# Kernel optimization log

Measured on AMD Instinct MI355X. Metric: run time of the kernel, lower is better.

Reference implementation:

```python
import jax, jax.numpy as jnp
import numpy as np

PI = jnp.pi


def _spow(t, p):
    # t >= 0; safe t**p with value 0 (and zero grad) at t == 0
    tt = jnp.where(t > 0, t, 1.0)
    return jnp.where(t > 0, tt ** p, 0.0)


def _wavelets(t, f, fm, pm, em, fo, ph):
    # t: [L]; f: [S,1] -> returns [S, L] bank of wavelets (one per scale)
    sigma = jnp.maximum(fm / (2.0 * PI * f), 1e-6)        # [S,1]
    br = jnp.cos(2.0 * PI * f * t)                        # [S,L]
    bi = jnp.sin(2.0 * PI * f * t)
    # real_part: + pm0*br - c^2 (t/sig)^fo0 br pm1 + ... alternating, c = 2..7
    real = br * pm[0]
    sign = -1.0
    for j in range(6):
        c = j + 2.0
        real = real + sign * (_spow(t, fo[j]) * c / sigma ** fo[j] * c) * br * pm[j + 1]
        sign = -sign
    # imag_part: same pattern with fo6..fo11, pm8..pm13; j==9 term has the
    # anomalous parenthesization from the source: t**fo*5/(sigma**fo*5)
    imag = bi * pm[7]
    sign = -1.0
    for j in range(6, 12):
        c = j - 4.0
        if j == 9:
            term = (_spow(t, fo[j]) * 5.0 / (sigma ** fo[j] * 5.0)) * bi * pm[j + 2]
        else:
            term = (_spow(t, fo[j]) * c / sigma ** fo[j] * c) * bi * pm[j + 2]
        imag = imag + sign * term
        sign = -sign
    gauss = em[0] * jnp.exp(-t ** 2 / (2.0 * sigma ** 2))  # [S,L]
    rw = real * gauss
    iw = imag * gauss
    amp = rw + iw
    samp = amp / jnp.linalg.norm(amp, axis=-1, keepdims=True)
    phase = jnp.arctan2(iw, rw)
    w = (samp * jnp.sin(phase) * ph[0]) * (samp * jnp.cos(phase) * ph[1]) \
        * (samp * jnp.sinc(phase / PI) * ph[2])
    return w


def reference(x, scales, f_mod, poly_mod, exp_mod, frac_order, phase_mod, i):
    B, C = x.shape[0], x.shape[1]
    xf = x.reshape(B, C, -1)                              # [B,C,L]
    L = xf.shape[-1]
    S = scales.shape[0]
    t = jnp.arange(L, dtype=x.dtype)
    f = (1.0 / scales)[:, None]                           # [S,1]
    W = _wavelets(t, f, f_mod[i], poly_mod[i], exp_mod[i], frac_order[i],
                  phase_mod[i])                            # [S,L] kernels, K = L
    # torch F.conv1d(padding='same', groups=C*S) = cross-correlation with
    # left pad (K-1)//2. Computed exactly via zero-padded FFT linear conv.
    K = L
    Nfft = 2 * L                                          # >= L + K - 1, no aliasing
    Xf = jnp.fft.rfft(xf, n=Nfft, axis=-1)                # [B,C,F]
    Wf = jnp.fft.rfft(W[:, ::-1], n=Nfft, axis=-1)        # [S,F] (corr = conv w/ flip)
    y = jnp.fft.irfft(Xf[:, :, None, :] * Wf[None, None], n=Nfft, axis=-1)  # [B,C,S,2L]
    left = (K - 1) // 2
    off = K - 1 - left
    y = y[..., off:off + L]                               # [B,C,S,L]
    # torch channel layout: out[:, j] = corr(x[:, j % C], wavelet[j % S])
    j = jnp.arange(C * S)
    return y[:, j % C, j % S, :]                          # [B, C*S, L]


def setup_inputs() -> dict:
    key = jax.random.key(0)
    ks = jax.random.split(key, 6)
    B, C, H, Wd = 16, 16, 64, 64
    S, NSTEPS = 16, 10
    x = jax.random.normal(ks[0], (B, C, H, Wd), dtype=jnp.float32)
    scales = jnp.linspace(1.0, 32.0, S, dtype=jnp.float32)
    f_mod = 1.0 + 0.02 * jax.random.normal(ks[1], (NSTEPS,), dtype=jnp.float32)
    poly_mod = 1.0 + 0.02 * jax.random.normal(ks[2], (NSTEPS, 14), dtype=jnp.float32)
    exp_mod = 1.0 + 0.02 * jax.random.normal(ks[3], (NSTEPS, 1), dtype=jnp.float32)
    frac_order = 1.0 + 0.02 * jax.random.normal(ks[4], (NSTEPS, 12), dtype=jnp.float32)
    phase_mod = 1.0 + 0.02 * jax.random.normal(ks[5], (NSTEPS, 3), dtype=jnp.float32)
    return {"x": x, "scales": scales, "f_mod": f_mod, "poly_mod": poly_mod,
            "exp_mod": exp_mod, "frac_order": frac_order,
            "phase_mod": phase_mod, "i": 3}
```

## Files before the change

kernel.cpp:

```cpp
#include <hip/hip_runtime.h>
#include <math.h>

#define QMAX 128
#define ZCUT 1920
#define PAD  131

__global__ void wavelet_build(const float* __restrict__ scales,
                              const float* __restrict__ f_mod,
                              const float* __restrict__ poly_mod,
                              const float* __restrict__ exp_mod,
                              const float* __restrict__ frac_order,
                              const float* __restrict__ phase_mod,
                              const int* __restrict__ istep,
                              float* __restrict__ Wout) {
    const int k = blockIdx.x;
    const int t = threadIdx.x;
    const int i = istep[0];
    const float PI2 = 6.28318530717958647692f;

    const float scale = scales[k];
    const float f = 1.0f / scale;
    const float fm = f_mod[i];
    const float* pm = poly_mod + i * 14;
    const float em0 = exp_mod[i];
    const float* fo = frac_order + i * 12;
    const float* ph = phase_mod + i * 3;

    const float sigma = fmaxf(fm / (PI2 * f), 1e-6f);
    const float tf = (float)t;
    const float arg = PI2 * f * tf;
    const float br = cosf(arg);
    const float bi = sinf(arg);

    float rp = pm[0];
    float sign = -1.0f;
    for (int j = 0; j < 6; ++j) {
        float c = (float)(j + 2);
        float sp = (tf > 0.0f) ? powf(tf, fo[j]) : 0.0f;
        float term = sp * c / powf(sigma, fo[j]) * c * pm[j + 1];
        rp += sign * term;
        sign = -sign;
    }
    float ipoly = pm[7];
    sign = -1.0f;
    for (int j = 6; j < 12; ++j) {
        float sp = (tf > 0.0f) ? powf(tf, fo[j]) : 0.0f;
        float term;
        if (j == 9) {
            term = sp * 5.0f / (powf(sigma, fo[j]) * 5.0f) * pm[j + 2];
        } else {
            float c = (float)(j - 4);
            term = sp * c / powf(sigma, fo[j]) * c * pm[j + 2];
        }
        ipoly += sign * term;
        sign = -sign;
    }

    const float gauss = em0 * expf(-tf * tf / (2.0f * sigma * sigma));
    const float rw = br * rp * gauss;
    const float iw = bi * ipoly * gauss;
    const float amp = rw + iw;

    float sq = amp * amp;
    #pragma unroll
    for (int off = 32; off > 0; off >>= 1) sq += __shfl_xor(sq, off, 64);
    __shared__ float wsum[2];
    if ((t & 63) == 0) wsum[t >> 6] = sq;
    __syncthreads();
    const float norm = sqrtf(wsum[0] + wsum[1]);

    const float samp = amp / norm;
    const float phase = atan2f(iw, rw);
    const float sphi = sinf(phase);
    const float cphi = cosf(phase);
    const float snc = (phase != 0.0f) ? (sphi / phase) : 1.0f;
    const float w = (samp * sphi * ph[0]) * (samp * cphi * ph[1]) * (samp * snc * ph[2]);
    Wout[k * QMAX + t] = w;
}

__global__ __launch_bounds__(256) void conv_diag(const float* __restrict__ x,
                                                 const float* __restrict__ W,
                                                 float* __restrict__ out) {
    __shared__ __attribute__((aligned(16))) float xs[PAD + 4096];
    __shared__ __attribute__((aligned(16))) float Wl[QMAX];

    const int bk = blockIdx.x;
    const int b = bk >> 4;
    const int k = bk & 15;
    const int tid = threadIdx.x;

    if (tid < QMAX) Wl[tid] = W[k * QMAX + tid];
    const float* xrow = x + (size_t)bk * 4096;
    for (int li = tid; li < PAD + 4096; li += 256) {
        xs[li] = (li >= PAD) ? xrow[li - PAD] : 0.0f;
    }
    __syncthreads();

    float* orow = out + ((size_t)b * 256 + k) * 4096;

    #pragma unroll
    for (int v = 0; v < 4; ++v) {
        const int fidx = tid + 256 * v;
        const int p = 4 * fidx;
        float4 val = make_float4(0.0f, 0.0f, 0.0f, 0.0f);
        if (p >= ZCUT) {
            float acc[4] = {0.0f, 0.0f, 0.0f, 0.0f};
            const int base = PAD + p - 2047;
            for (int q = 0; q < QMAX; q += 4) {
                float4 w4 = *(const float4*)&Wl[q];
                float4 x0 = *(const float4*)&xs[base + q];
                float4 x1 = *(const float4*)&xs[base + q + 4];
                float win[8] = {x0.x, x0.y, x0.z, x0.w,
                                x1.x, x1.y, x1.z, x1.w};
                float wv[4] = {w4.x, w4.y, w4.z, w4.w};
                #pragma unroll
                for (int j = 0; j < 4; ++j) {
                    #pragma unroll
                    for (int r = 0; r < 4; ++r) {
                        acc[r] = fmaf(win[r + j], wv[j], acc[r]);
                    }
                }
            }
            val = make_float4(acc[0], acc[1], acc[2], acc[3]);
        }
        *(float4*)&orow[p] = val;
    }
}

__global__ __launch_bounds__(256) void replicate_rows(float* __restrict__ out) {
    const int k = blockIdx.z;
    const int rr = blockIdx.y;
    const int b = blockIdx.x;
    const int r = 1 + (rr & 15);
    const float* src = out + ((size_t)b * 256 + k) * 4096;
    float* dst = out + ((size_t)b * 256 + (size_t)(rr + 1) * 16 + k) * 4096;
    const int tid = threadIdx.x;
    (void)r;
    #pragma unroll
    for (int v = 0; v < 4; ++v) {
        const int fidx = tid + 256 * v;
        float4 val = *(const float4*)&src[4 * fidx];
        __builtin_nontemporal_store(val.x, &dst[4 * fidx + 0]);
        __builtin_nontemporal_store(val.y, &dst[4 * fidx + 1]);
        __builtin_nontemporal_store(val.z, &dst[4 * fidx + 2]);
        __builtin_nontemporal_store(val.w, &dst[4 * fidx + 3]);
    }
}

extern "C" void kernel_launch(void* const* d_in, const int* in_sizes, int n_in,
                              void* d_out, int out_size, void* d_ws, size_t ws_size,
                              hipStream_t stream) {
    const float* x          = (const float*)d_in[0];
    const float* scales     = (const float*)d_in[1];
    const float* f_mod      = (const float*)d_in[2];
    const float* poly_mod   = (const float*)d_in[3];
    const float* exp_mod    = (const float*)d_in[4];
    const float* frac_order = (const float*)d_in[5];
    const float* phase_mod  = (const float*)d_in[6];
    const int*   istep      = (const int*)d_in[7];
    float* out = (float*)d_out;
    float* Wbuf = (float*)d_ws;

    wavelet_build<<<dim3(16), dim3(QMAX), 0, stream>>>(
        scales, f_mod, poly_mod, exp_mod, frac_order, phase_mod, istep, Wbuf);

    conv_diag<<<dim3(256), dim3(256), 0, stream>>>(x, Wbuf, out);

    replicate_rows<<<dim3(16, 15, 16), dim3(256), 0, stream>>>(out);
}
```

Measured before the change: 40.37 us.

## Fuse wavelet construction into conv kernel and trim shared-memory input staging

Removes the separate wavelet_build launch: each conv block now computes its own 128-tap wavelet in shared memory before the convolution. The shared x buffer is cut to the 2176 samples actually read, which shrinks the global load and LDS footprint. The replicate kernel switches to a 1D grid and a single vector nontemporal store per float4. The cost is redundant wavelet math repeated in every block, plus one extra barrier.

```diff
diff --git a/kernel.cpp b/kernel.cpp
--- a/kernel.cpp
+++ b/kernel.cpp
@@ -3,109 +3,108 @@
 
 #define QMAX 128
 #define ZCUT 1920
-#define PAD  131
+#define XPAD 127
+#define XLEN 2176
+#define XS_SZ 2304
 
-__global__ void wavelet_build(const float* __restrict__ scales,
-                              const float* __restrict__ f_mod,
-                              const float* __restrict__ poly_mod,
-                              const float* __restrict__ exp_mod,
-                              const float* __restrict__ frac_order,
-                              const float* __restrict__ phase_mod,
-                              const int* __restrict__ istep,
-                              float* __restrict__ Wout) {
-    const int k = blockIdx.x;
-    const int t = threadIdx.x;
-    const int i = istep[0];
-    const float PI2 = 6.28318530717958647692f;
-
-    const float scale = scales[k];
-    const float f = 1.0f / scale;
-    const float fm = f_mod[i];
-    const float* pm = poly_mod + i * 14;
-    const float em0 = exp_mod[i];
-    const float* fo = frac_order + i * 12;
-    const float* ph = phase_mod + i * 3;
-
-    const float sigma = fmaxf(fm / (PI2 * f), 1e-6f);
-    const float tf = (float)t;
-    const float arg = PI2 * f * tf;
-    const float br = cosf(arg);
-    const float bi = sinf(arg);
-
-    float rp = pm[0];
-    float sign = -1.0f;
-    for (int j = 0; j < 6; ++j) {
-        float c = (float)(j + 2);
-        float sp = (tf > 0.0f) ? powf(tf, fo[j]) : 0.0f;
-        float term = sp * c / powf(sigma, fo[j]) * c * pm[j + 1];
-        rp += sign * term;
-        sign = -sign;
-    }
-    float ipoly = pm[7];
-    sign = -1.0f;
-    for (int j = 6; j < 12; ++j) {
-        float sp = (tf > 0.0f) ? powf(tf, fo[j]) : 0.0f;
-        float term;
-        if (j == 9) {
-            term = sp * 5.0f / (powf(sigma, fo[j]) * 5.0f) * pm[j + 2];
-        } else {
-            float c = (float)(j - 4);
-            term = sp * c / powf(sigma, fo[j]) * c * pm[j + 2];
-        }
-        ipoly += sign * term;
-        sign = -sign;
-    }
-
-    const float gauss = em0 * expf(-tf * tf / (2.0f * sigma * sigma));
-    const float rw = br * rp * gauss;
-    const float iw = bi * ipoly * gauss;
-    const float amp = rw + iw;
-
-    float sq = amp * amp;
-    #pragma unroll
-    for (int off = 32; off > 0; off >>= 1) sq += __shfl_xor(sq, off, 64);
-    __shared__ float wsum[2];
-    if ((t & 63) == 0) wsum[t >> 6] = sq;
-    __syncthreads();
-    const float norm = sqrtf(wsum[0] + wsum[1]);
-
-    const float samp = amp / norm;
-    const float phase = atan2f(iw, rw);
-    const float sphi = sinf(phase);
-    const float cphi = cosf(phase);
-    const float snc = (phase != 0.0f) ? (sphi / phase) : 1.0f;
-    const float w = (samp * sphi * ph[0]) * (samp * cphi * ph[1]) * (samp * snc * ph[2]);
-    Wout[k * QMAX + t] = w;
-}
+typedef float vfloat4 __attribute__((ext_vector_type(4)));
 
 __global__ __launch_bounds__(256) void conv_diag(const float* __restrict__ x,
-                                                 const float* __restrict__ W,
+                                                 const float* __restrict__ scales,
+                                                 const float* __restrict__ f_mod,
+                                                 const float* __restrict__ poly_mod,
+                                                 const float* __restrict__ exp_mod,
+                                                 const float* __restrict__ frac_order,
+                                                 const float* __restrict__ phase_mod,
+                                                 const int* __restrict__ istep,
                                                  float* __restrict__ out) {
-    __shared__ __attribute__((aligned(16))) float xs[PAD + 4096];
+    __shared__ __attribute__((aligned(16))) float xs[XS_SZ];
     __shared__ __attribute__((aligned(16))) float Wl[QMAX];
+    __shared__ float wsum[2];
 
     const int bk = blockIdx.x;
     const int b = bk >> 4;
     const int k = bk & 15;
     const int tid = threadIdx.x;
 
-    if (tid < QMAX) Wl[tid] = W[k * QMAX + tid];
     const float* xrow = x + (size_t)bk * 4096;
-    for (int li = tid; li < PAD + 4096; li += 256) {
-        xs[li] = (li >= PAD) ? xrow[li - PAD] : 0.0f;
+    for (int li = tid; li < XS_SZ; li += 256) {
+        xs[li] = (li >= XPAD && li < XPAD + XLEN) ? xrow[li - XPAD] : 0.0f;
+    }
+
+    float amp = 0.0f, rw = 0.0f, iw = 0.0f;
+    if (tid < QMAX) {
+        const int i = istep[0];
+        const float PI2 = 6.28318530717958647692f;
+        const float f = 1.0f / scales[k];
+        const float fm = f_mod[i];
+        const float* pm = poly_mod + i * 14;
+        const float em0 = exp_mod[i];
+        const float* fo = frac_order + i * 12;
+
+        const float sigma = fmaxf(fm / (PI2 * f), 1e-6f);
+        const float tf = (float)tid;
+        const float arg = PI2 * f * tf;
+        const float br = cosf(arg);
+        const float bi = sinf(arg);
+
+        float rp = pm[0];
+        float sign = -1.0f;
+        for (int j = 0; j < 6; ++j) {
+            float c = (float)(j + 2);
+            float sp = (tf > 0.0f) ? powf(tf, fo[j]) : 0.0f;
+            float term = sp * c / powf(sigma, fo[j]) * c * pm[j + 1];
+            rp += sign * term;
+            sign = -sign;
+        }
+        float ipoly = pm[7];
+        sign = -1.0f;
+        for (int j = 6; j < 12; ++j) {
+            float sp = (tf > 0.0f) ? powf(tf, fo[j]) : 0.0f;
+            float term;
+            if (j == 9) {
+                term = sp * 5.0f / (powf(sigma, fo[j]) * 5.0f) * pm[j + 2];
+            } else {
+                float c = (float)(j - 4);
+                term = sp * c / powf(sigma, fo[j]) * c * pm[j + 2];
+            }
+            ipoly += sign * term;
+            sign = -sign;
+        }
+
+        const float gauss = em0 * expf(-tf * tf / (2.0f * sigma * sigma));
+        rw = br * rp * gauss;
+        iw = bi * ipoly * gauss;
+        amp = rw + iw;
+
+        float sq = amp * amp;
+        #pragma unroll
+        for (int off = 32; off > 0; off >>= 1) sq += __shfl_xor(sq, off, 64);
+        if ((tid & 63) == 0) wsum[tid >> 6] = sq;
+    }
+    __syncthreads();
+
+    if (tid < QMAX) {
+        const int i = istep[0];
+        const float* ph = phase_mod + i * 3;
+        const float norm = sqrtf(wsum[0] + wsum[1]);
+        const float samp = amp / norm;
+        const float phase = atan2f(iw, rw);
+        const float sphi = sinf(phase);
+        const float cphi = cosf(phase);
+        const float snc = (phase != 0.0f) ? (sphi / phase) : 1.0f;
+        Wl[tid] = (samp * sphi * ph[0]) * (samp * cphi * ph[1]) * (samp * snc * ph[2]);
     }
     __syncthreads();
 
     float* orow = out + ((size_t)b * 256 + k) * 4096;
-
     #pragma unroll
     for (int v = 0; v < 4; ++v) {
-        const int fidx = tid + 256 * v;
-        const int p = 4 * fidx;
+        const int p = 4 * (tid + 256 * v);
         float4 val = make_float4(0.0f, 0.0f, 0.0f, 0.0f);
         if (p >= ZCUT) {
             float acc[4] = {0.0f, 0.0f, 0.0f, 0.0f};
-            const int base = PAD + p - 2047;
+            const int base = p - 1920;
             for (int q = 0; q < QMAX; q += 4) {
                 float4 w4 = *(const float4*)&Wl[q];
                 float4 x0 = *(const float4*)&xs[base + q];
@@ -128,22 +127,18 @@
 }
 
 __global__ __launch_bounds__(256) void replicate_rows(float* __restrict__ out) {
-    const int k = blockIdx.z;
-    const int rr = blockIdx.y;
-    const int b = blockIdx.x;
-    const int r = 1 + (rr & 15);
-    const float* src = out + ((size_t)b * 256 + k) * 4096;
-    float* dst = out + ((size_t)b * 256 + (size_t)(rr + 1) * 16 + k) * 4096;
+    const int blk = blockIdx.x;
+    const int b = blk / 240;
+    const int j = 16 + (blk - b * 240);
+    const int k = j & 15;
+    const float* __restrict__ src = out + ((size_t)b * 256 + k) * 4096;
+    float* __restrict__ dst = out + ((size_t)b * 256 + j) * 4096;
     const int tid = threadIdx.x;
-    (void)r;
     #pragma unroll
     for (int v = 0; v < 4; ++v) {
-        const int fidx = tid + 256 * v;
-        float4 val = *(const float4*)&src[4 * fidx];
-        __builtin_nontemporal_store(val.x, &dst[4 * fidx + 0]);
-        __builtin_nontemporal_store(val.y, &dst[4 * fidx + 1]);
-        __builtin_nontemporal_store(val.z, &dst[4 * fidx + 2]);
-        __builtin_nontemporal_store(val.w, &dst[4 * fidx + 3]);
+        const int e = 4 * (tid + 256 * v);
+        vfloat4 val = *(const vfloat4*)&src[e];
+        __builtin_nontemporal_store(val, (vfloat4*)&dst[e]);
     }
 }
 
@@ -159,12 +154,9 @@
     const float* phase_mod  = (const float*)d_in[6];
     const int*   istep      = (const int*)d_in[7];
     float* out = (float*)d_out;
-    float* Wbuf = (float*)d_ws;
 
-    wavelet_build<<<dim3(16), dim3(QMAX), 0, stream>>>(
-        scales, f_mod, poly_mod, exp_mod, frac_order, phase_mod, istep, Wbuf);
+    conv_diag<<<dim3(256), dim3(256), 0, stream>>>(
+        x, scales, f_mod, poly_mod, exp_mod, frac_order, phase_mod, istep, out);
 
-    conv_diag<<<dim3(256), dim3(256), 0, stream>>>(x, Wbuf, out);
-
-    replicate_rows<<<dim3(16, 15, 16), dim3(256), 0, stream>>>(out);
+    replicate_rows<<<dim3(3840), dim3(256), 0, stream>>>(out);
 }
```

After: 35.76 us. 11.4% less time.
